# Kernel optimization log

Measured on AMD Instinct MI355X. Metric: run time of the kernel, lower is better.

## Reference

```python
import jax, jax.numpy as jnp
import numpy as np

NA, NT, NG = 100000, 300000, 2000        # artist / track / genre node counts
EPT, ETG = 600000, 400000                # performed / has_genre edge counts
IN_A, IN_T, IN_G = 64, 96, 32            # raw feature dims per node type
HID, HEADS, OUT, L = 64, 4, 64, 2        # GATv2 per-head dim = HID, concat=False
NEG_SLOPE = 0.2                          # GATv2 LeakyReLU slope


def setup_inputs() -> dict:
    key = jax.random.key(0)
    ks = jax.random.split(key, 32)
    f = lambda k, s, sc: jax.random.normal(k, s, dtype=jnp.float32) * sc
    z = lambda s: jnp.zeros(s, dtype=jnp.float32)
    return {
        "x_artist": f(ks[0], (NA, IN_A), 1.0),
        "x_track": f(ks[1], (NT, IN_T), 1.0),
        "x_genre": f(ks[2], (NG, IN_G), 1.0),
        "enc_Wa": f(ks[3], (IN_A, HID), 0.05), "enc_ba": z((HID,)),
        "enc_Wt": f(ks[4], (IN_T, HID), 0.05), "enc_bt": z((HID,)),
        "enc_Wg": f(ks[5], (IN_G, HID), 0.05), "enc_bg": z((HID,)),
        "src_pt": jax.random.randint(ks[6], (EPT,), 0, NA, dtype=jnp.int32),
        "dst_pt": jax.random.randint(ks[7], (EPT,), 0, NT, dtype=jnp.int32),
        "src_tg": jax.random.randint(ks[8], (ETG,), 0, NT, dtype=jnp.int32),
        "dst_tg": jax.random.randint(ks[9], (ETG,), 0, NG, dtype=jnp.int32),
        "Wl_pt": f(ks[10], (L, HID, HEADS, HID), 0.05), "bl_pt": z((L, HEADS, HID)),
        "Wr_pt": f(ks[11], (L, HID, HEADS, HID), 0.05), "br_pt": z((L, HEADS, HID)),
        "att_pt": f(ks[12], (L, HEADS, HID), 0.05), "bias_pt": z((L, HID)),
        "Wl_tg": f(ks[13], (L, HID, HEADS, HID), 0.05), "bl_tg": z((L, HEADS, HID)),
        "Wr_tg": f(ks[14], (L, HID, HEADS, HID), 0.05), "br_tg": z((L, HEADS, HID)),
        "att_tg": f(ks[15], (L, HEADS, HID), 0.05), "bias_tg": z((L, HID)),
        "lin_track_W": f(ks[16], (HID, OUT), 0.05), "lin_track_b": z((OUT,)),
        "lin_genre_W": f(ks[17], (HID, OUT), 0.05), "lin_genre_b": z((OUT,)),
    }


def _gatv2(xs, xd, src, dst, Wl, bl, Wr, br, att, bias, n_dst):
    """Bipartite GATv2Conv, heads averaged (concat=False), no self loops, eval mode."""
    gl = jnp.einsum("nd,dhc->nhc", xs, Wl) + bl            # [Ns,H,C] src transform
    gr = jnp.einsum("nd,dhc->nhc", xd, Wr) + br            # [Nd,H,C] dst transform
    e = jax.nn.leaky_relu(gl[src] + gr[dst], NEG_SLOPE)    # [E,H,C]
    s = jnp.einsum("ehc,hc->eh", e, att)                   # [E,H] logits
    m = jax.ops.segment_max(s, dst, num_segments=n_dst)    # per-dst softmax (stable)
    m = jnp.where(jnp.isfinite(m), m, 0.0)
    ex = jnp.exp(s - m[dst])
    den = jax.ops.segment_sum(ex, dst, num_segments=n_dst)
    alpha = ex / (den[dst] + 1e-16)                        # [E,H]
    out = jax.ops.segment_sum(gl[src] * alpha[:, :, None], dst, num_segments=n_dst)
    return out.mean(axis=1) + bias                         # [Nd,C]


def _l2norm(x):
    n = jnp.sqrt(jnp.sum(x * x, axis=-1, keepdims=True))
    return x / jnp.maximum(n, 1e-12)


def reference(x_artist, x_track, x_genre, enc_Wa, enc_ba, enc_Wt, enc_bt, enc_Wg, enc_bg,
              src_pt, dst_pt, src_tg, dst_tg,
              Wl_pt, bl_pt, Wr_pt, br_pt, att_pt, bias_pt,
              Wl_tg, bl_tg, Wr_tg, br_tg, att_tg, bias_tg,
              lin_track_W, lin_track_b, lin_genre_W, lin_genre_b):
    enc_a = x_artist @ enc_Wa + enc_ba
    enc_t = x_track @ enc_Wt + enc_bt
    enc_g = x_genre @ enc_Wg + enc_bg
    # Faithful to source: every layer reads the encoder output (hidden never fed back),
    # so only the last layer's weights determine the result.
    for l in range(L):
        h_track = jax.nn.elu(_gatv2(enc_a, enc_t, src_pt, dst_pt,
                                    Wl_pt[l], bl_pt[l], Wr_pt[l], br_pt[l],
                                    att_pt[l], bias_pt[l], NT))
        h_genre = jax.nn.elu(_gatv2(enc_t, enc_g, src_tg, dst_tg,
                                    Wl_tg[l], bl_tg[l], Wr_tg[l], br_tg[l],
                                    att_tg[l], bias_tg[l], NG))
    out_track = _l2norm(h_track @ lin_track_W + lin_track_b)
    out_genre = _l2norm(h_genre @ lin_genre_W + lin_genre_b)
    return out_track, out_genre
```

## Files before the change

### kernel.cpp

```cpp
#include <hip/hip_runtime.h>
#include <hip/hip_bf16.h>

typedef __hip_bfloat16 bf16;
typedef __attribute__((ext_vector_type(8))) short short8;
typedef __attribute__((ext_vector_type(4))) float f32x4;

#define NA 100000
#define NT 300000
#define NG 2000
#define EPT 600000
#define ETG 400000

#define DSB 64
#define DBK 64

#define DPP_QX1 0xB1
#define DPP_QX2 0x4E
#define DPP_RR4 0x124
#define DPP_RR8 0x128

template <int CTRL>
__device__ __forceinline__ float dppadd(float x) {
    int y = __builtin_amdgcn_update_dpp(0, __float_as_int(x), CTRL, 0xf, 0xf, true);
    return x + __int_as_float(y);
}

__device__ __forceinline__ float b2f(short s) {
    return __uint_as_float(((unsigned)(unsigned short)s) << 16);
}
__device__ __forceinline__ void cvt16(short8 a, short8 b, float* f) {
#pragma unroll
    for (int j = 0; j < 8; ++j) f[j] = b2f(a[j]);
#pragma unroll
    for (int j = 0; j < 8; ++j) f[8 + j] = b2f(b[j]);
}
__device__ __forceinline__ short f2bs(float x) {
    return (short)__builtin_bit_cast(unsigned short, __float2bfloat16(x));
}

__global__ void fill_u32(unsigned* __restrict__ p, unsigned v, long n) {
    long i = (long)blockIdx.x * 256 + threadIdx.x;
    if (i < n) p[i] = v;
}

__global__ __launch_bounds__(256) void wprep(
    const float* __restrict__ We, const float* __restrict__ Wl,
    const float* __restrict__ bl, const float* __restrict__ be,
    short* __restrict__ Bf, float* __restrict__ bc, int KS)
{
    int t = blockIdx.x * 256 + threadIdx.x;
    if (t < KS * 1024) {
        int c = t & 15, kb = (t >> 4) & 3, nt = (t >> 6) & 15, ks = t >> 10;
        int k0 = ks * 32 + kb * 8, n = nt * 16 + c;
        short8 o;
#pragma unroll
        for (int j = 0; j < 8; ++j) {
            int k = k0 + j;
            float acc = 0.f;
            for (int cc = 0; cc < 64; ++cc)
                acc = fmaf(We[k * 64 + cc], Wl[cc * 256 + n], acc);
            o[j] = f2bs(acc);
        }
        ((short8*)Bf)[t] = o;
    }
    if (blockIdx.x == 0) {
        int j = threadIdx.x;
        float acc = bl[j];
        for (int cc = 0; cc < 64; ++cc) acc = fmaf(be[cc], Wl[cc * 256 + j], acc);
        bc[j] = acc;
    }
}

template <int KS>
__global__ __launch_bounds__(256) void tformf(
    const float* __restrict__ A, const short* __restrict__ Bf,
    const float* __restrict__ bias, bf16* __restrict__ C, int M)
{
    constexpr int K = KS * 32;
    int wv = threadIdx.x >> 6, lane = threadIdx.x & 63;
    int lrow = lane & 15, kb = lane >> 4;
    int base = blockIdx.x * 64 + wv * 16;

    int arow = base + lrow; if (arow >= M) arow = M - 1;
    const float* Ap = A + (size_t)arow * K + kb * 8;
    short8 a[KS];
#pragma unroll
    for (int s = 0; s < KS; ++s) {
        f32x4 lo = *(const f32x4*)(Ap + s * 32);
        f32x4 hi = *(const f32x4*)(Ap + s * 32 + 4);
#pragma unroll
        for (int j = 0; j < 4; ++j) {
            a[s][j]     = f2bs(lo[j]);
            a[s][4 + j] = f2bs(hi[j]);
        }
    }

    const short8* Bl = (const short8*)Bf + kb * 16 + lrow;

    f32x4 acc[16];
#pragma unroll
    for (int nt = 0; nt < 16; ++nt) {
        float bv = bias[nt * 16 + lrow];
        f32x4 bvv = {bv, bv, bv, bv};
        acc[nt] = bvv;
    }
#pragma unroll
    for (int nt = 0; nt < 16; ++nt) {
#pragma unroll
        for (int s = 0; s < KS; ++s)
            acc[nt] = __builtin_amdgcn_mfma_f32_16x16x32_bf16(
                a[s], Bl[(s * 16 + nt) * 64], acc[nt], 0, 0, 0);
    }
    int r0 = base + kb * 4;
#pragma unroll
    for (int nt = 0; nt < 16; ++nt) {
#pragma unroll
        for (int r = 0; r < 4; ++r) {
            int row = r0 + r;
            if (row < M)
                C[(size_t)row * 256 + nt * 16 + lrow] = __float2bfloat16(acc[nt][r]);
        }
    }
}

__global__ __launch_bounds__(256) void histo(
    const int* __restrict__ dst, unsigned* __restrict__ cnt, int base, int E)
{
    int i = blockIdx.x * 256 + threadIdx.x;
    if (i < E) atomicAdd(&cnt[base + dst[i]], 1u);
}

__global__ __launch_bounds__(256) void scan_a(
    const unsigned* __restrict__ in, unsigned* __restrict__ out,
    unsigned* __restrict__ part, int n)
{
    __shared__ unsigned ts[256];
    int t = threadIdx.x;
    long base = (long)blockIdx.x * 1024 + (long)t * 4;
    unsigned v0 = 0, v1 = 0, v2 = 0, v3 = 0;
    if (base + 0 < n) v0 = in[base + 0];
    if (base + 1 < n) v1 = in[base + 1];
    if (base + 2 < n) v2 = in[base + 2];
    if (base + 3 < n) v3 = in[base + 3];
    unsigned s = v0 + v1 + v2 + v3;
    ts[t] = s;
    __syncthreads();
    unsigned run = s;
    for (int off = 1; off < 256; off <<= 1) {
        unsigned y = (t >= off) ? ts[t - off] : 0u;
        __syncthreads();
        run += y; ts[t] = run;
        __syncthreads();
    }
    unsigned ex = run - s;
    if (base + 0 < n) out[base + 0] = ex;
    if (base + 1 < n) out[base + 1] = ex + v0;
    if (base + 2 < n) out[base + 2] = ex + v0 + v1;
    if (base + 3 < n) out[base + 3] = ex + v0 + v1 + v2;
    if (t == 255) part[blockIdx.x] = run;
}

__global__ __launch_bounds__(256) void scan_c(
    unsigned* __restrict__ rp, const unsigned* __restrict__ part,
    unsigned* __restrict__ cur, int n)
{
    long i = (long)blockIdx.x * 256 + threadIdx.x;
    if (i >= n) return;
    unsigned v = rp[i] + part[i >> 10];
    rp[i] = v;
    if (i < n - 1) cur[i] = v;
}

__global__ __launch_bounds__(256) void scat(
    const int* __restrict__ src, const int* __restrict__ dst,
    unsigned* __restrict__ cur, int base, int* __restrict__ ss, int E)
{
    int i = blockIdx.x * 256 + threadIdx.x;
    if (i < E) {
        unsigned p = atomicAdd(&cur[base + dst[i]], 1u);
        ss[p] = src[i];
    }
}

__global__ __launch_bounds__(256) void deg_cnt(
    const unsigned* __restrict__ rp, unsigned* __restrict__ bcnt, int n)
{
    __shared__ unsigned hcnt[DBK];
    int b = blockIdx.x;
    int chunk = (n + DSB - 1) / DSB;
    int lo = b * chunk, hi = min(n, lo + chunk);
    if (threadIdx.x < DBK) hcnt[threadIdx.x] = 0u;
    __syncthreads();
    for (int i = lo + threadIdx.x; i < hi; i += 256) {
        unsigned deg = rp[i + 1] - rp[i];
        if (deg > DBK - 1) deg = DBK - 1;
        atomicAdd(&hcnt[deg], 1u);
    }
    __syncthreads();
    if (threadIdx.x < DBK) bcnt[(size_t)threadIdx.x * DSB + b] = hcnt[threadIdx.x];
}

__global__ __launch_bounds__(256) void scan4k(
    const unsigned* __restrict__ in, unsigned* __restrict__ out)
{
    __shared__ unsigned ts[256];
    int t = threadIdx.x;
    unsigned v[16]; unsigned s = 0;
#pragma unroll
    for (int j = 0; j < 16; ++j) { v[j] = in[t * 16 + j]; s += v[j]; }
    ts[t] = s;
    __syncthreads();
    unsigned run = s;
    for (int off = 1; off < 256; off <<= 1) {
        unsigned y = (t >= off) ? ts[t - off] : 0u;
        __syncthreads();
        run += y; ts[t] = run;
        __syncthreads();
    }
    unsigned ex = run - s;
#pragma unroll
    for (int j = 0; j < 16; ++j) { out[t * 16 + j] = ex; ex += v[j]; }
}

__global__ __launch_bounds__(256) void deg_place(
    const unsigned* __restrict__ rp, const unsigned* __restrict__ base,
    int* __restrict__ order, int n)
{
    __shared__ unsigned hcur[DBK];
    int b = blockIdx.x;
    int chunk = (n + DSB - 1) / DSB;
    int lo = b * chunk, hi = min(n, lo + chunk);
    if (threadIdx.x < DBK) hcur[threadIdx.x] = base[(size_t)threadIdx.x * DSB + b];
    __syncthreads();
    for (int i = lo + threadIdx.x; i < hi; i += 256) {
        unsigned deg = rp[i + 1] - rp[i];
        if (deg > DBK - 1) deg = DBK - 1;
        unsigned p = atomicAdd(&hcur[deg], 1u);
        order[p] = i;
    }
}

__global__ __launch_bounds__(256) void gat_w(
    const bf16* __restrict__ gl, const bf16* __restrict__ gr,
    const int* __restrict__ ssrc, const unsigned* __restrict__ rp,
    const int* __restrict__ order,
    const float* __restrict__ att, const float* __restrict__ bias,
    const float* __restrict__ linW, const float* __restrict__ linb,
    float* __restrict__ outp, int Nd)
{
    __shared__ float WL[4096];
    __shared__ float bL[64];
    __shared__ float hC[64];
    __shared__ float hL[16][68];
    for (int t = threadIdx.x; t < 4096; t += 256) WL[t] = linW[t];
    if (threadIdx.x < 64) {
        float b = bias[threadIdx.x];
        bL[threadIdx.x] = b;
        hC[threadIdx.x] = b > 0.f ? b : (__expf(b) - 1.f);
    }
    __syncthreads();

    int grp = threadIdx.x >> 4, g = threadIdx.x & 15;
    int h = g & 3, q = g >> 2;
    int eoff = h * 64 + q * 16;

    float at[16];
#pragma unroll
    for (int j = 0; j < 16; ++j) at[j] = att[eoff + j];
    f32x4 lbv = *(const f32x4*)(linb + g * 4);

    f32x4 ycn;
    {
        float y0 = lbv[0], y1 = lbv[1], y2 = lbv[2], y3 = lbv[3];
#pragma unroll
        for (int c = 0; c < 64; c += 4) {
            f32x4 hv = *(const f32x4*)&hC[c];
            const float* wr = WL + c * 64 + g * 4;
            f32x4 w0 = *(const f32x4*)(wr);
            f32x4 w1 = *(const f32x4*)(wr + 64);
            f32x4 w2 = *(const f32x4*)(wr + 128);
            f32x4 w3 = *(const f32x4*)(wr + 192);
            y0 = fmaf(hv[0], w0[0], y0); y1 = fmaf(hv[0], w0[1], y1);
            y2 = fmaf(hv[0], w0[2], y2); y3 = fmaf(hv[0], w0[3], y3);
            y0 = fmaf(hv[1], w1[0], y0); y1 = fmaf(hv[1], w1[1], y1);
            y2 = fmaf(hv[1], w1[2], y2); y3 = fmaf(hv[1], w1[3], y3);
            y0 = fmaf(hv[2], w2[0], y0); y1 = fmaf(hv[2], w2[1], y1);
            y2 = fmaf(hv[2], w2[2], y2); y3 = fmaf(hv[2], w2[3], y3);
            y0 = fmaf(hv[3], w3[0], y0); y1 = fmaf(hv[3], w3[1], y1);
            y2 = fmaf(hv[3], w3[2], y2); y3 = fmaf(hv[3], w3[3], y3);
        }
        float ss = y0 * y0 + y1 * y1 + y2 * y2 + y3 * y3;
        ss = dppadd<DPP_QX1>(ss);
        ss = dppadd<DPP_QX2>(ss);
        ss = dppadd<DPP_RR4>(ss);
        ss = dppadd<DPP_RR8>(ss);
        float rn = 1.f / fmaxf(sqrtf(ss), 1e-12f);
        ycn[0] = y0 * rn; ycn[1] = y1 * rn; ycn[2] = y2 * rn; ycn[3] = y3 * rn;
    }

    long ngroups = (Nd + 15) >> 4;
    for (long it = blockIdx.x; it < ngroups; it += gridDim.x) {
        long idx = it * 16 + grp;
        if (idx >= Nd) continue;
        int d = order[idx];
        unsigned beg = rp[d], end = rp[d + 1];
        if (beg == end) {
            *(f32x4*)(outp + (size_t)d * 64 + g * 4) = ycn;
            continue;
        }
        const short* grow = (const short*)gr + (size_t)d * 256 + eoff;
        short8 gr0 = *(const short8*)grow;
        short8 gr1 = *(const short8*)(grow + 8);
        float grf[16];
        cvt16(gr0, gr1, grf);

        float den = 0.f;
        float acc[16];
#pragma unroll
        for (int j = 0; j < 16; ++j) acc[j] = 0.f;

        unsigned e = beg;
        {
            int si = ssrc[e];
            const short* p0 = (const short*)gl + (size_t)si * 256 + eoff;
            short8 gA = *(const short8*)p0;
            short8 gB = *(const short8*)(p0 + 8);
            while (true) {
                float glf[16];
                cvt16(gA, gB, glf);
                ++e;
                bool more = e < end;
                if (more) {
                    int s2 = ssrc[e];
                    const short* p2 = (const short*)gl + (size_t)s2 * 256 + eoff;
                    gA = *(const short8*)p2;
                    gB = *(const short8*)(p2 + 8);
                }
                float pd = 0.f;
#pragma unroll
                for (int j = 0; j < 16; ++j) {
                    float v = glf[j] + grf[j];
                    float lr = fmaxf(v, 0.2f * v);
                    pd = fmaf(lr, at[j], pd);
                }
                pd = dppadd<DPP_RR4>(pd);
                pd = dppadd<DPP_RR8>(pd);
                float w = __expf(pd);
                den += w;
#pragma unroll
                for (int j = 0; j < 16; ++j) acc[j] = fmaf(w, glf[j], acc[j]);
                if (!more) break;
            }
        }
        float inv = 1.f / den;

        float x[16];
#pragma unroll
        for (int j = 0; j < 16; ++j) {
            float v = acc[j] * inv;
            v = dppadd<DPP_QX1>(v);
            v = dppadd<DPP_QX2>(v);
            x[j] = v;
        }
#pragma unroll
        for (int j = 0; j < 16; ++j) {
            float v = fmaf(0.25f, x[j], bL[q * 16 + j]);
            x[j] = v > 0.f ? v : (__expf(v) - 1.f);
        }
        if (h == 0) {
#pragma unroll
            for (int j = 0; j < 16; ++j) hL[grp][q * 16 + j] = x[j];
        }
        __builtin_amdgcn_wave_barrier();

        float y0 = lbv[0], y1 = lbv[1], y2 = lbv[2], y3 = lbv[3];
#pragma unroll
        for (int c = 0; c < 64; c += 4) {
            f32x4 hv = *(const f32x4*)&hL[grp][c];
            const float* wr = WL + c * 64 + g * 4;
            f32x4 w0 = *(const f32x4*)(wr);
            f32x4 w1 = *(const f32x4*)(wr + 64);
            f32x4 w2 = *(const f32x4*)(wr + 128);
            f32x4 w3 = *(const f32x4*)(wr + 192);
            y0 = fmaf(hv[0], w0[0], y0); y1 = fmaf(hv[0], w0[1], y1);
            y2 = fmaf(hv[0], w0[2], y2); y3 = fmaf(hv[0], w0[3], y3);
            y0 = fmaf(hv[1], w1[0], y0); y1 = fmaf(hv[1], w1[1], y1);
            y2 = fmaf(hv[1], w1[2], y2); y3 = fmaf(hv[1], w1[3], y3);
            y0 = fmaf(hv[2], w2[0], y0); y1 = fmaf(hv[2], w2[1], y1);
            y2 = fmaf(hv[2], w2[2], y2); y3 = fmaf(hv[2], w2[3], y3);
            y0 = fmaf(hv[3], w3[0], y0); y1 = fmaf(hv[3], w3[1], y1);
            y2 = fmaf(hv[3], w3[2], y2); y3 = fmaf(hv[3], w3[3], y3);
        }
        float ss = y0 * y0 + y1 * y1 + y2 * y2 + y3 * y3;
        ss = dppadd<DPP_QX1>(ss);
        ss = dppadd<DPP_QX2>(ss);
        ss = dppadd<DPP_RR4>(ss);
        ss = dppadd<DPP_RR8>(ss);
        float rn = 1.f / fmaxf(sqrtf(ss), 1e-12f);
        f32x4 yo = {y0 * rn, y1 * rn, y2 * rn, y3 * rn};
        *(f32x4*)(outp + (size_t)d * 64 + g * 4) = yo;
    }
}

__global__ __launch_bounds__(256) void gat_b(
    const bf16* __restrict__ gl, const bf16* __restrict__ gr,
    const int* __restrict__ ssrc, const unsigned* __restrict__ rp,
    const float* __restrict__ att, const float* __restrict__ bias,
    const float* __restrict__ linW, const float* __restrict__ linb,
    float* __restrict__ outp, int Nd)
{
    __shared__ float accL[16][256];
    __shared__ float denL[16][4];
    int grp = threadIdx.x >> 4, g = threadIdx.x & 15;
    int h = g & 3, q = g >> 2;
    int eoff = h * 64 + q * 16;
    int d = blockIdx.x;

    float at[16];
#pragma unroll
    for (int j = 0; j < 16; ++j) at[j] = att[eoff + j];

    const short* grow = (const short*)gr + (size_t)d * 256 + eoff;
    short8 gr0 = *(const short8*)grow;
    short8 gr1 = *(const short8*)(grow + 8);
    float grf[16];
    cvt16(gr0, gr1, grf);

    unsigned beg = rp[d], end = rp[d + 1];
    float den = 0.f;
    float acc[16];
#pragma unroll
    for (int j = 0; j < 16; ++j) acc[j] = 0.f;

    unsigned e = beg + grp;
    if (e < end) {
        int si = ssrc[e];
        const short* p0 = (const short*)gl + (size_t)si * 256 + eoff;
        short8 gA = *(const short8*)p0;
        short8 gB = *(const short8*)(p0 + 8);
        while (true) {
            float glf[16];
            cvt16(gA, gB, glf);
            e += 16;
            bool more = e < end;
            if (more) {
                int s2 = ssrc[e];
                const short* p2 = (const short*)gl + (size_t)s2 * 256 + eoff;
                gA = *(const short8*)p2;
                gB = *(const short8*)(p2 + 8);
            }
            float pd = 0.f;
#pragma unroll
            for (int j = 0; j < 16; ++j) {
                float v = glf[j] + grf[j];
                float lr = fmaxf(v, 0.2f * v);
                pd = fmaf(lr, at[j], pd);
            }
            pd = dppadd<DPP_RR4>(pd);
            pd = dppadd<DPP_RR8>(pd);
            float w = __expf(pd);
            den += w;
#pragma unroll
            for (int j = 0; j < 16; ++j) acc[j] = fmaf(w, glf[j], acc[j]);
            if (!more) break;
        }
    }
#pragma unroll
    for (int j = 0; j < 16; ++j) accL[grp][eoff + j] = acc[j];
    if (q == 0) denL[grp][h] = den;
    __syncthreads();

    int t = threadIdx.x;
    int hh = t >> 6, cc = t & 63;
    float sa = 0.f, sd = 0.f;
#pragma unroll
    for (int k = 0; k < 16; ++k) { sa += accL[k][hh * 64 + cc]; sd += denL[k][hh]; }
    float xv = sd > 0.f ? sa / sd : 0.f;
    __syncthreads();
    accL[0][t] = xv;
    __syncthreads();
    if (t < 64) {
        float m4 = 0.25f * (accL[0][t] + accL[0][64 + t] + accL[0][128 + t] + accL[0][192 + t]);
        float v = m4 + bias[t];
        accL[1][t] = v > 0.f ? v : (__expf(v) - 1.f);
    }
    __syncthreads();
    if (t < 64) {
        float y = linb[t];
        for (int c = 0; c < 64; ++c) y = fmaf(accL[1][c], linW[c * 64 + t], y);
        float ss = y * y;
        ss += __shfl_xor(ss, 1);  ss += __shfl_xor(ss, 2);  ss += __shfl_xor(ss, 4);
        ss += __shfl_xor(ss, 8);  ss += __shfl_xor(ss, 16); ss += __shfl_xor(ss, 32);
        float rn = 1.f / fmaxf(sqrtf(ss), 1e-12f);
        outp[(size_t)d * 64 + t] = y * rn;
    }
}


static inline unsigned gridFor(long n) { return (unsigned)((n + 255) / 256); }

extern "C" void kernel_launch(void* const* d_in, const int* in_sizes, int n_in,
                              void* d_out, int out_size, void* d_ws, size_t ws_size,
                              hipStream_t stream) {
    const float* x_artist = (const float*)d_in[0];
    const float* x_track  = (const float*)d_in[1];
    const float* x_genre  = (const float*)d_in[2];
    const float* enc_Wa = (const float*)d_in[3];  const float* enc_ba = (const float*)d_in[4];
    const float* enc_Wt = (const float*)d_in[5];  const float* enc_bt = (const float*)d_in[6];
    const float* enc_Wg = (const float*)d_in[7];  const float* enc_bg = (const float*)d_in[8];
    const int* src_pt = (const int*)d_in[9];
    const int* dst_pt = (const int*)d_in[10];
    const int* src_tg = (const int*)d_in[11];
    const int* dst_tg = (const int*)d_in[12];
    const float* Wl_pt   = (const float*)d_in[13] + 64 * 256;
    const float* bl_pt   = (const float*)d_in[14] + 256;
    const float* Wr_pt   = (const float*)d_in[15] + 64 * 256;
    const float* br_pt   = (const float*)d_in[16] + 256;
    const float* att_pt  = (const float*)d_in[17] + 256;
    const float* bias_pt = (const float*)d_in[18] + 64;
    const float* Wl_tg   = (const float*)d_in[19] + 64 * 256;
    const float* bl_tg   = (const float*)d_in[20] + 256;
    const float* Wr_tg   = (const float*)d_in[21] + 64 * 256;
    const float* br_tg   = (const float*)d_in[22] + 256;
    const float* att_tg  = (const float*)d_in[23] + 256;
    const float* bias_tg = (const float*)d_in[24] + 64;
    const float* lin_track_W = (const float*)d_in[25];
    const float* lin_track_b = (const float*)d_in[26];
    const float* lin_genre_W = (const float*)d_in[27];
    const float* lin_genre_b = (const float*)d_in[28];

    float* out = (float*)d_out;

    const int NTOT = NT + NG;

    char* p = (char*)d_ws;
    auto take = [&](size_t bytes) { char* q = p; p += (bytes + 255) & ~(size_t)255; return q; };
    char* region = take((size_t)NA * 256 * 2 + (size_t)NT * 256 * 2);
    bf16*  gl_pt  = (bf16*)region;
    bf16*  gr_pt  = (bf16*)(region + (size_t)NA * 256 * 2);
    bf16*  gl_tg  = (bf16*)region;
    unsigned* counts = (unsigned*)take((size_t)(NTOT + 1) * 4);
    unsigned* rowptr = (unsigned*)take((size_t)(NTOT + 1) * 4);
    unsigned* cursor = (unsigned*)take((size_t)NTOT * 4);
    unsigned* part   = (unsigned*)take((size_t)2048 * 4);
    int*      ssrc   = (int*)take((size_t)(EPT + ETG) * 4);
    int*      order  = (int*)take((size_t)NT * 4);
    unsigned* bcnt   = (unsigned*)take((size_t)DBK * DSB * 4);
    unsigned* bbase  = (unsigned*)take((size_t)DBK * DSB * 4);
    bf16*     gr_tg  = (bf16*)take((size_t)NG * 256 * 2);
    short*    Bf     = (short*)take((size_t)(64 + 96 + 96 + 32) * 256 * 2);
    float*    bc     = (float*)take((size_t)4 * 256 * 4);

    short* BfGLpt = Bf;
    short* BfGRpt = BfGLpt + 64 * 256;
    short* BfGLtg = BfGRpt + 96 * 256;
    short* BfGRtg = BfGLtg + 96 * 256;
    float* bcGLpt = bc;
    float* bcGRpt = bc + 256;
    float* bcGLtg = bc + 512;
    float* bcGRtg = bc + 768;

    dim3 blk(256);

    wprep<<<8,  blk, 0, stream>>>(enc_Wa, Wl_pt, bl_pt, enc_ba, BfGLpt, bcGLpt, 2);
    wprep<<<12, blk, 0, stream>>>(enc_Wt, Wr_pt, br_pt, enc_bt, BfGRpt, bcGRpt, 3);
    wprep<<<12, blk, 0, stream>>>(enc_Wt, Wl_tg, bl_tg, enc_bt, BfGLtg, bcGLtg, 3);
    wprep<<<4,  blk, 0, stream>>>(enc_Wg, Wr_tg, br_tg, enc_bg, BfGRtg, bcGRtg, 1);

    {
        int n = NTOT + 1;
        unsigned sgrid = (unsigned)((n + 1023) / 1024);
        fill_u32<<<gridFor(n), blk, 0, stream>>>(counts, 0u, n);
        histo<<<gridFor(EPT), blk, 0, stream>>>(dst_pt, counts, 0, EPT);
        histo<<<gridFor(ETG), blk, 0, stream>>>(dst_tg, counts, NT, ETG);
        scan_a<<<sgrid, blk, 0, stream>>>(counts, rowptr, part, n);
        scan_a<<<1, blk, 0, stream>>>(part, part, part + 1536, (int)sgrid);
        scan_c<<<gridFor(n), blk, 0, stream>>>(rowptr, part, cursor, n);
        scat<<<gridFor(EPT), blk, 0, stream>>>(src_pt, dst_pt, cursor, 0, ssrc, EPT);
        scat<<<gridFor(ETG), blk, 0, stream>>>(src_tg, dst_tg, cursor, NT, ssrc, ETG);
    }

    deg_cnt  <<<DSB, blk, 0, stream>>>(rowptr, bcnt, NT);
    scan4k   <<<1,   blk, 0, stream>>>(bcnt, bbase);
    deg_place<<<DSB, blk, 0, stream>>>(rowptr, bbase, order, NT);

    tformf<2><<<(NA + 63) / 64, blk, 0, stream>>>(x_artist, BfGLpt, bcGLpt, gl_pt, NA);
    tformf<3><<<(NT + 63) / 64, blk, 0, stream>>>(x_track,  BfGRpt, bcGRpt, gr_pt, NT);

    gat_w<<<2048, blk, 0, stream>>>(gl_pt, gr_pt, ssrc, rowptr, order, att_pt, bias_pt,
                                    lin_track_W, lin_track_b, out, NT);

    tformf<3><<<(NT + 63) / 64, blk, 0, stream>>>(x_track, BfGLtg, bcGLtg, gl_tg, NT);
    tformf<1><<<(NG + 63) / 64, blk, 0, stream>>>(x_genre, BfGRtg, bcGRtg, gr_tg, NG);

    gat_b<<<NG, blk, 0, stream>>>(gl_tg, gr_tg, ssrc, rowptr + NT, att_tg, bias_tg,
                                  lin_genre_W, lin_genre_b, out + (size_t)NT * 64, NG);
}
```

Measured before the change: 864.0 us.

## Merge setup launches, fuse dual track transforms, use exp2 softmax

Merges the four weight-prep launches, the two histogram launches and the two scatter launches into single kernels. When the workspace is large enough, it gives the track-side gl_tg its own buffer and computes gr_pt and gl_tg in one pass over x_track, which saves a second read of the 300k-row input and a launch. The attention vector is pre-scaled by log2(e) so the softmax weight can use exp2f instead of __expf. The cost is extra workspace for the unaliased buffer, plus a size-dependent branch that falls back to the old schedule.

```diff
diff --git a/kernel.cpp b/kernel.cpp
--- a/kernel.cpp
+++ b/kernel.cpp
@@ -13,6 +13,7 @@
 
 #define DSB 64
 #define DBK 64
+#define LOG2E 1.44269504088896f
 
 #define DPP_QX1 0xB1
 #define DPP_QX2 0x4E
@@ -43,13 +44,15 @@
     if (i < n) p[i] = v;
 }
 
-__global__ __launch_bounds__(256) void wprep(
-    const float* __restrict__ We, const float* __restrict__ Wl,
-    const float* __restrict__ bl, const float* __restrict__ be,
-    short* __restrict__ Bf, float* __restrict__ bc, int KS)
-{
-    int t = blockIdx.x * 256 + threadIdx.x;
-    if (t < KS * 1024) {
+struct WP { const float *We, *Wl, *bl, *be; short* Bf; float* bc; int KS, b0; };
+
+__global__ __launch_bounds__(256) void wprep_all(WP p0, WP p1, WP p2, WP p3) {
+    int b = blockIdx.x;
+    WP p;
+    if (b < 8) p = p0; else if (b < 20) p = p1; else if (b < 32) p = p2; else p = p3;
+    int lb = b - p.b0;
+    int t = lb * 256 + threadIdx.x;
+    if (t < p.KS * 1024) {
         int c = t & 15, kb = (t >> 4) & 3, nt = (t >> 6) & 15, ks = t >> 10;
         int k0 = ks * 32 + kb * 8, n = nt * 16 + c;
         short8 o;
@@ -58,16 +61,16 @@
             int k = k0 + j;
             float acc = 0.f;
             for (int cc = 0; cc < 64; ++cc)
-                acc = fmaf(We[k * 64 + cc], Wl[cc * 256 + n], acc);
+                acc = fmaf(p.We[k * 64 + cc], p.Wl[cc * 256 + n], acc);
             o[j] = f2bs(acc);
         }
-        ((short8*)Bf)[t] = o;
-    }
-    if (blockIdx.x == 0) {
+        ((short8*)p.Bf)[t] = o;
+    }
+    if (lb == 0) {
         int j = threadIdx.x;
-        float acc = bl[j];
-        for (int cc = 0; cc < 64; ++cc) acc = fmaf(be[cc], Wl[cc * 256 + j], acc);
-        bc[j] = acc;
+        float acc = p.bl[j];
+        for (int cc = 0; cc < 64; ++cc) acc = fmaf(p.be[cc], p.Wl[cc * 256 + j], acc);
+        p.bc[j] = acc;
     }
 }
 
@@ -123,11 +126,104 @@
     }
 }
 
-__global__ __launch_bounds__(256) void histo(
-    const int* __restrict__ dst, unsigned* __restrict__ cnt, int base, int E)
+__global__ __launch_bounds__(256) void tformf2(
+    const float* __restrict__ A,
+    const short* __restrict__ Bf1, const float* __restrict__ b1, bf16* __restrict__ C1,
+    const short* __restrict__ Bf2, const float* __restrict__ b2, bf16* __restrict__ C2,
+    int M)
+{
+    constexpr int KS = 3, K = 96;
+    int wv = threadIdx.x >> 6, lane = threadIdx.x & 63;
+    int lrow = lane & 15, kb = lane >> 4;
+    int base = blockIdx.x * 64 + wv * 16;
+
+    int arow = base + lrow; if (arow >= M) arow = M - 1;
+    const float* Ap = A + (size_t)arow * K + kb * 8;
+    short8 a[KS];
+#pragma unroll
+    for (int s = 0; s < KS; ++s) {
+        f32x4 lo = *(const f32x4*)(Ap + s * 32);
+        f32x4 hi = *(const f32x4*)(Ap + s * 32 + 4);
+#pragma unroll
+        for (int j = 0; j < 4; ++j) {
+            a[s][j]     = f2bs(lo[j]);
+            a[s][4 + j] = f2bs(hi[j]);
+        }
+    }
+    int r0 = base + kb * 4;
+
+    const short8* Bl1 = (const short8*)Bf1 + kb * 16 + lrow;
+    f32x4 acc[16];
+#pragma unroll
+    for (int nt = 0; nt < 16; ++nt) {
+        float bv = b1[nt * 16 + lrow];
+        f32x4 bvv = {bv, bv, bv, bv};
+        acc[nt] = bvv;
+    }
+#pragma unroll
+    for (int nt = 0; nt < 16; ++nt) {
+#pragma unroll
+        for (int s = 0; s < KS; ++s)
+            acc[nt] = __builtin_amdgcn_mfma_f32_16x16x32_bf16(
+                a[s], Bl1[(s * 16 + nt) * 64], acc[nt], 0, 0, 0);
+    }
+#pragma unroll
+    for (int nt = 0; nt < 16; ++nt) {
+#pragma unroll
+        for (int r = 0; r < 4; ++r) {
+            int row = r0 + r;
+            if (row < M)
+                C1[(size_t)row * 256 + nt * 16 + lrow] = __float2bfloat16(acc[nt][r]);
+        }
+    }
+
+    const short8* Bl2 = (const short8*)Bf2 + kb * 16 + lrow;
+#pragma unroll
+    for (int nt = 0; nt < 16; ++nt) {
+        float bv = b2[nt * 16 + lrow];
+        f32x4 bvv = {bv, bv, bv, bv};
+        acc[nt] = bvv;
+    }
+#pragma unroll
+    for (int nt = 0; nt < 16; ++nt) {
+#pragma unroll
+        for (int s = 0; s < KS; ++s)
+            acc[nt] = __builtin_amdgcn_mfma_f32_16x16x32_bf16(
+                a[s], Bl2[(s * 16 + nt) * 64], acc[nt], 0, 0, 0);
+    }
+#pragma unroll
+    for (int nt = 0; nt < 16; ++nt) {
+#pragma unroll
+        for (int r = 0; r < 4; ++r) {
+            int row = r0 + r;
+            if (row < M)
+                C2[(size_t)row * 256 + nt * 16 + lrow] = __float2bfloat16(acc[nt][r]);
+        }
+    }
+}
+
+__global__ __launch_bounds__(256) void histo_all(
+    const int* __restrict__ dpt, const int* __restrict__ dtg,
+    unsigned* __restrict__ cnt)
 {
     int i = blockIdx.x * 256 + threadIdx.x;
-    if (i < E) atomicAdd(&cnt[base + dst[i]], 1u);
+    if (i < EPT) atomicAdd(&cnt[dpt[i]], 1u);
+    else if (i < EPT + ETG) atomicAdd(&cnt[NT + dtg[i - EPT]], 1u);
+}
+
+__global__ __launch_bounds__(256) void scat_all(
+    const int* __restrict__ spt, const int* __restrict__ dpt,
+    const int* __restrict__ stg, const int* __restrict__ dtg,
+    unsigned* __restrict__ cur, int* __restrict__ ss)
+{
+    int i = blockIdx.x * 256 + threadIdx.x;
+    if (i < EPT) {
+        unsigned p = atomicAdd(&cur[dpt[i]], 1u);
+        ss[p] = spt[i];
+    } else if (i < EPT + ETG) {
+        unsigned p = atomicAdd(&cur[NT + dtg[i - EPT]], 1u);
+        ss[p] = stg[i - EPT];
+    }
 }
 
 __global__ __launch_bounds__(256) void scan_a(
@@ -171,17 +267,6 @@
     if (i < n - 1) cur[i] = v;
 }
 
-__global__ __launch_bounds__(256) void scat(
-    const int* __restrict__ src, const int* __restrict__ dst,
-    unsigned* __restrict__ cur, int base, int* __restrict__ ss, int E)
-{
-    int i = blockIdx.x * 256 + threadIdx.x;
-    if (i < E) {
-        unsigned p = atomicAdd(&cur[base + dst[i]], 1u);
-        ss[p] = src[i];
-    }
-}
-
 __global__ __launch_bounds__(256) void deg_cnt(
     const unsigned* __restrict__ rp, unsigned* __restrict__ bcnt, int n)
 {
@@ -266,7 +351,7 @@
 
     float at[16];
 #pragma unroll
-    for (int j = 0; j < 16; ++j) at[j] = att[eoff + j];
+    for (int j = 0; j < 16; ++j) at[j] = att[eoff + j] * LOG2E;
     f32x4 lbv = *(const f32x4*)(linb + g * 4);
 
     f32x4 ycn;
@@ -345,7 +430,7 @@
                 }
                 pd = dppadd<DPP_RR4>(pd);
                 pd = dppadd<DPP_RR8>(pd);
-                float w = __expf(pd);
+                float w = exp2f(pd);
                 den += w;
 #pragma unroll
                 for (int j = 0; j < 16; ++j) acc[j] = fmaf(w, glf[j], acc[j]);
@@ -418,7 +503,7 @@
 
     float at[16];
 #pragma unroll
-    for (int j = 0; j < 16; ++j) at[j] = att[eoff + j];
+    for (int j = 0; j < 16; ++j) at[j] = att[eoff + j] * LOG2E;
 
     const short* grow = (const short*)gr + (size_t)d * 256 + eoff;
     short8 gr0 = *(const short8*)grow;
@@ -458,7 +543,7 @@
             }
             pd = dppadd<DPP_RR4>(pd);
             pd = dppadd<DPP_RR8>(pd);
-            float w = __expf(pd);
+            float w = exp2f(pd);
             den += w;
 #pragma unroll
             for (int j = 0; j < 16; ++j) acc[j] = fmaf(w, glf[j], acc[j]);
@@ -533,12 +618,33 @@
 
     const int NTOT = NT + NG;
 
+    const size_t smallBytes =
+        ((size_t)(NTOT + 1) * 4 + 255 & ~(size_t)255) * 2 +
+        ((size_t)NTOT * 4 + 255 & ~(size_t)255) +
+        8192 +
+        ((size_t)(EPT + ETG) * 4) +
+        ((size_t)NT * 4 + 255 & ~(size_t)255) +
+        16384 * 2 +
+        (size_t)NG * 512 +
+        (size_t)(64 + 96 + 96 + 32) * 512 +
+        4096 + 65536;
+    const size_t needFused = (size_t)NA * 512 + (size_t)NT * 512 * 2 + smallBytes;
+    bool fused = ws_size >= needFused;
+
     char* p = (char*)d_ws;
     auto take = [&](size_t bytes) { char* q = p; p += (bytes + 255) & ~(size_t)255; return q; };
-    char* region = take((size_t)NA * 256 * 2 + (size_t)NT * 256 * 2);
-    bf16*  gl_pt  = (bf16*)region;
-    bf16*  gr_pt  = (bf16*)(region + (size_t)NA * 256 * 2);
-    bf16*  gl_tg  = (bf16*)region;
+
+    bf16 *gl_pt, *gr_pt, *gl_tg;
+    if (fused) {
+        gl_pt = (bf16*)take((size_t)NA * 256 * 2);
+        gr_pt = (bf16*)take((size_t)NT * 256 * 2);
+        gl_tg = (bf16*)take((size_t)NT * 256 * 2);
+    } else {
+        char* region = take((size_t)NA * 256 * 2 + (size_t)NT * 256 * 2);
+        gl_pt = (bf16*)region;
+        gr_pt = (bf16*)(region + (size_t)NA * 256 * 2);
+        gl_tg = (bf16*)region;
+    }
     unsigned* counts = (unsigned*)take((size_t)(NTOT + 1) * 4);
     unsigned* rowptr = (unsigned*)take((size_t)(NTOT + 1) * 4);
     unsigned* cursor = (unsigned*)take((size_t)NTOT * 4);
@@ -562,37 +668,49 @@
 
     dim3 blk(256);
 
-    wprep<<<8,  blk, 0, stream>>>(enc_Wa, Wl_pt, bl_pt, enc_ba, BfGLpt, bcGLpt, 2);
-    wprep<<<12, blk, 0, stream>>>(enc_Wt, Wr_pt, br_pt, enc_bt, BfGRpt, bcGRpt, 3);
-    wprep<<<12, blk, 0, stream>>>(enc_Wt, Wl_tg, bl_tg, enc_bt, BfGLtg, bcGLtg, 3);
-    wprep<<<4,  blk, 0, stream>>>(enc_Wg, Wr_tg, br_tg, enc_bg, BfGRtg, bcGRtg, 1);
+    WP p0 = {enc_Wa, Wl_pt, bl_pt, enc_ba, BfGLpt, bcGLpt, 2, 0};
+    WP p1 = {enc_Wt, Wr_pt, br_pt, enc_bt, BfGRpt, bcGRpt, 3, 8};
+    WP p2 = {enc_Wt, Wl_tg, bl_tg, enc_bt, BfGLtg, bcGLtg, 3, 20};
+    WP p3 = {enc_Wg, Wr_tg, br_tg, enc_bg, BfGRtg, bcGRtg, 1, 32};
+    wprep_all<<<36, blk, 0, stream>>>(p0, p1, p2, p3);
 
     {
         int n = NTOT + 1;
         unsigned sgrid = (unsigned)((n + 1023) / 1024);
         fill_u32<<<gridFor(n), blk, 0, stream>>>(counts, 0u, n);
-        histo<<<gridFor(EPT), blk, 0, stream>>>(dst_pt, counts, 0, EPT);
-        histo<<<gridFor(ETG), blk, 0, stream>>>(dst_tg, counts, NT, ETG);
+        histo_all<<<gridFor(EPT + ETG), blk, 0, stream>>>(dst_pt, dst_tg, counts);
         scan_a<<<sgrid, blk, 0, stream>>>(counts, rowptr, part, n);
         scan_a<<<1, blk, 0, stream>>>(part, part, part + 1536, (int)sgrid);
         scan_c<<<gridFor(n), blk, 0, stream>>>(rowptr, part, cursor, n);
-        scat<<<gridFor(EPT), blk, 0, stream>>>(src_pt, dst_pt, cursor, 0, ssrc, EPT);
-        scat<<<gridFor(ETG), blk, 0, stream>>>(src_tg, dst_tg, cursor, NT, ssrc, ETG);
+        scat_all<<<gridFor(EPT + ETG), blk, 0, stream>>>(src_pt, dst_pt, src_tg, dst_tg,
+                                                         cursor, ssrc);
     }
 
     deg_cnt  <<<DSB, blk, 0, stream>>>(rowptr, bcnt, NT);
     scan4k   <<<1,   blk, 0, stream>>>(bcnt, bbase);
     deg_place<<<DSB, blk, 0, stream>>>(rowptr, bbase, order, NT);
 
-    tformf<2><<<(NA + 63) / 64, blk, 0, stream>>>(x_artist, BfGLpt, bcGLpt, gl_pt, NA);
-    tformf<3><<<(NT + 63) / 64, blk, 0, stream>>>(x_track,  BfGRpt, bcGRpt, gr_pt, NT);
-
-    gat_w<<<2048, blk, 0, stream>>>(gl_pt, gr_pt, ssrc, rowptr, order, att_pt, bias_pt,
-                                    lin_track_W, lin_track_b, out, NT);
-
-    tformf<3><<<(NT + 63) / 64, blk, 0, stream>>>(x_track, BfGLtg, bcGLtg, gl_tg, NT);
-    tformf<1><<<(NG + 63) / 64, blk, 0, stream>>>(x_genre, BfGRtg, bcGRtg, gr_tg, NG);
-
-    gat_b<<<NG, blk, 0, stream>>>(gl_tg, gr_tg, ssrc, rowptr + NT, att_tg, bias_tg,
-                                  lin_genre_W, lin_genre_b, out + (size_t)NT * 64, NG);
-}
+    if (fused) {
+        tformf<2><<<(NA + 63) / 64, blk, 0, stream>>>(x_artist, BfGLpt, bcGLpt, gl_pt, NA);
+        tformf2  <<<(NT + 63) / 64, blk, 0, stream>>>(x_track, BfGRpt, bcGRpt, gr_pt,
+                                                      BfGLtg, bcGLtg, gl_tg, NT);
+        tformf<1><<<(NG + 63) / 64, blk, 0, stream>>>(x_genre, BfGRtg, bcGRtg, gr_tg, NG);
+
+        gat_w<<<2048, blk, 0, stream>>>(gl_pt, gr_pt, ssrc, rowptr, order, att_pt, bias_pt,
+                                        lin_track_W, lin_track_b, out, NT);
+        gat_b<<<NG, blk, 0, stream>>>(gl_tg, gr_tg, ssrc, rowptr + NT, att_tg, bias_tg,
+                                      lin_genre_W, lin_genre_b, out + (size_t)NT * 64, NG);
+    } else {
+        tformf<2><<<(NA + 63) / 64, blk, 0, stream>>>(x_artist, BfGLpt, bcGLpt, gl_pt, NA);
+        tformf<3><<<(NT + 63) / 64, blk, 0, stream>>>(x_track,  BfGRpt, bcGRpt, gr_pt, NT);
+
+        gat_w<<<2048, blk, 0, stream>>>(gl_pt, gr_pt, ssrc, rowptr, order, att_pt, bias_pt,
+                                        lin_track_W, lin_track_b, out, NT);
+
+        tformf<3><<<(NT + 63) / 64, blk, 0, stream>>>(x_track, BfGLtg, bcGLtg, gl_tg, NT);
+        tformf<1><<<(NG + 63) / 64, blk, 0, stream>>>(x_genre, BfGRtg, bcGRtg, gr_tg, NG);
+
+        gat_b<<<NG, blk, 0, stream>>>(gl_tg, gr_tg, ssrc, rowptr + NT, att_tg, bias_tg,
+                                      lin_genre_W, lin_genre_b, out + (size_t)NT * 64, NG);
+    }
+}
```

Result: faster. 779.4 us (-9.8%).
